# Kernel tuning notes

Hardware: AMD Instinct MI355X
Metric: run time of the kernel (lower is better)

Reference implementation:

```python
import jax, jax.numpy as jnp
import numpy as np

B, N, E, HD = 4, 2048, 2048, 128
E2 = 2 * E
EPS = 1e-6


def setup_inputs() -> dict:
    key = jax.random.key(0)
    ks = jax.random.split(key, 7)
    s = 0.02  # init_std
    return {
        "x": jax.random.normal(ks[0], (B, N, E), dtype=jnp.float32),
        "Wq1": jax.random.normal(ks[1], (E, HD), dtype=jnp.float32) * s,
        "Wq2": jax.random.normal(ks[2], (HD, E2), dtype=jnp.float32) * s,
        "Wk1": jax.random.normal(ks[3], (E, HD), dtype=jnp.float32) * s,
        "Wk2": jax.random.normal(ks[4], (HD, E2), dtype=jnp.float32) * s,
        "Wv": jax.random.normal(ks[5], (E, E2), dtype=jnp.float32) * s,
        "Wo": jax.random.normal(ks[6], (E2, E), dtype=jnp.float32) * s,
        "norm_w": jnp.ones((E2,), dtype=jnp.float32),
    }


def reference(x, Wq1, Wq2, Wk1, Wk2, Wv, Wo, norm_w):
    # low-rank factored projections: embed -> head_dim -> 2*embed
    q = jax.nn.silu((x @ Wq1) @ Wq2)          # [B,N,2E]
    log_f_raw = (x @ Wk1) @ Wk2                # [B,N,2E]
    v = x @ Wv                                 # [B,N,2E]

    # faithful to source (lower_bound is None branch):
    # f = sigmoid(raw); log_f = logsigmoid(f); k = 1 - exp(log_f)
    f = jax.nn.sigmoid(log_f_raw)
    log_f = jax.nn.log_sigmoid(f)
    a = jnp.exp(log_f)                         # decay (forget gate)
    k = 1.0 - a                                # input gate

    # HGRN-1 elementwise gated recurrence: h_t = a_t*h_{t-1} + k_t*v_t
    def combine(c1, c2):
        a1, b1 = c1
        a2, b2 = c2
        return (a1 * a2, a2 * b1 + b2)

    _, h = jax.lax.associative_scan(combine, (a, k * v), axis=1)
    out = q * h                                # [B,N,2E]

    # RMSNorm over channel dim (2E)
    out = out * jax.lax.rsqrt(jnp.mean(out * out, axis=-1, keepdims=True) + EPS)
    out = out * norm_w

    return out @ Wo                            # [B,N,E]
```

## Files before the change

### kernel.cpp

```cpp
#include <hip/hip_runtime.h>


typedef unsigned short u16;
typedef __attribute__((ext_vector_type(4))) float f32x4;
typedef __attribute__((ext_vector_type(8))) __bf16 bf16x8;
typedef __attribute__((ext_vector_type(8))) u16 u16x8;
typedef __attribute__((ext_vector_type(4))) unsigned int u32x4;

__device__ __forceinline__ float bf2f(u16 u) {
  unsigned int i = ((unsigned int)u) << 16;
  return __builtin_bit_cast(float, i);
}
__device__ __forceinline__ u16 f2bf(float f) {
  unsigned int i = __builtin_bit_cast(unsigned int, f);
  i += 0x7fffu + ((i >> 16) & 1u);
  return (u16)(i >> 16);
}

__device__ __forceinline__ void gload_lds16(const u16* g, u16* l) {
  __builtin_amdgcn_global_load_lds(
      (const __attribute__((address_space(1))) void*)g,
      (__attribute__((address_space(3))) void*)l, 16, 0, 0);
}

__global__ __launch_bounds__(256) void cast_kernel(const float* __restrict__ in,
                                                   u16* __restrict__ out, long n) {
  long i = ((long)blockIdx.x * 256 + threadIdx.x) * 4;
  if (i >= n) return;
  f32x4 fv = *(const f32x4*)&in[i];
  unsigned long long pk = (unsigned long long)f2bf(fv[0]) |
                          ((unsigned long long)f2bf(fv[1]) << 16) |
                          ((unsigned long long)f2bf(fv[2]) << 32) |
                          ((unsigned long long)f2bf(fv[3]) << 48);
  *(unsigned long long*)&out[i] = pk;
}

__global__ __launch_bounds__(256) void transpose_cast(const float* __restrict__ W,
                                                      u16* __restrict__ WT, int R, int Cc) {
  __shared__ float tile[32][33];
  const int tx = threadIdx.x, ty = threadIdx.y;
  const int x = blockIdx.x * 32 + tx;
  const int ybase = blockIdx.y * 32;
#pragma unroll
  for (int i = 0; i < 32; i += 8)
    tile[ty + i][tx] = W[(size_t)(ybase + ty + i) * Cc + x];
  __syncthreads();
  const int xt = ybase + tx;
  const int ytbase = blockIdx.x * 32;
#pragma unroll
  for (int i = 0; i < 32; i += 8)
    WT[(size_t)(ytbase + ty + i) * R + xt] = f2bf(tile[tx][ty + i]);
}

__global__ __launch_bounds__(256) void transpose_cast_nw(const float* __restrict__ W,
                                                         const float* __restrict__ nw,
                                                         u16* __restrict__ WT, int R, int Cc) {
  __shared__ float tile[32][33];
  const int tx = threadIdx.x, ty = threadIdx.y;
  const int x = blockIdx.x * 32 + tx;
  const int ybase = blockIdx.y * 32;
#pragma unroll
  for (int i = 0; i < 32; i += 8)
    tile[ty + i][tx] = W[(size_t)(ybase + ty + i) * Cc + x];
  __syncthreads();
  const int xt = ybase + tx;
  const float s = nw[xt];
  const int ytbase = blockIdx.x * 32;
#pragma unroll
  for (int i = 0; i < 32; i += 8)
    WT[(size_t)(ytbase + ty + i) * R + xt] = f2bf(tile[tx][ty + i] * s);
}

template <int EPI>
__global__ __launch_bounds__(256) void gemm_bt(const u16* __restrict__ A, int lda,
                                               const u16* __restrict__ BT,
                                               void* __restrict__ Cv,
                                               int M, int N, int K) {
  __shared__ __align__(16) u16 As[4096];
  __shared__ __align__(16) u16 Bs[4096];
  const int tid = threadIdx.x;
  const int lane = tid & 63;
  const int wid = tid >> 6;
  const int wr = wid >> 1, wc = wid & 1;
  const long bm = (long)blockIdx.x * 128;
  const long bn = (long)blockIdx.y * 128;

  const int sm = lane >> 2;
  const int sk = (lane & 3) << 3;
  const u16* Ag0 = A + (size_t)(bm + wid * 16 + sm) * lda + sk;
  const u16* Ag1 = A + (size_t)(bm + 64 + wid * 16 + sm) * lda + sk;
  const u16* Bg0 = BT + (size_t)(bn + wid * 16 + sm) * K + sk;
  const u16* Bg1 = BT + (size_t)(bn + 64 + wid * 16 + sm) * K + sk;
  u16* As0 = As + wid * 512;
  u16* As1 = As + 2048 + wid * 512;
  u16* Bs0 = Bs + wid * 512;
  u16* Bs1 = Bs + 2048 + wid * 512;

  f32x4 acc[4][4] = {};

  const int fra = wr * 64 + (lane & 15);
  const int frb = wc * 64 + (lane & 15);
  const int kg = (lane >> 4) << 3;

  for (int kk = 0; kk < K; kk += 32) {
    gload_lds16(Ag0 + kk, As0);
    gload_lds16(Ag1 + kk, As1);
    gload_lds16(Bg0 + kk, Bs0);
    gload_lds16(Bg1 + kk, Bs1);
    __syncthreads();
    bf16x8 af[4], bv[4];
#pragma unroll
    for (int mi = 0; mi < 4; ++mi)
      af[mi] = *reinterpret_cast<const bf16x8*>(&As[(fra + mi * 16) * 32 + kg]);
#pragma unroll
    for (int ni = 0; ni < 4; ++ni)
      bv[ni] = *reinterpret_cast<const bf16x8*>(&Bs[(frb + ni * 16) * 32 + kg]);
#pragma unroll
    for (int mi = 0; mi < 4; ++mi) {
#pragma unroll
      for (int ni = 0; ni < 4; ++ni)
        acc[mi][ni] =
            __builtin_amdgcn_mfma_f32_16x16x32_bf16(af[mi], bv[ni], acc[mi][ni], 0, 0, 0);
    }
    __syncthreads();
  }

  const int r0 = wr * 64 + ((lane >> 4) << 2);
  const int c0 = wc * 64 + (lane & 15);
#pragma unroll
  for (int mi = 0; mi < 4; ++mi) {
#pragma unroll
    for (int ni = 0; ni < 4; ++ni) {
#pragma unroll
      for (int r = 0; r < 4; ++r) {
        size_t row = (size_t)(bm + r0 + mi * 16 + r);
        size_t col = (size_t)(bn + c0 + ni * 16);
        size_t idx = row * (size_t)N + col;
        float val = acc[mi][ni][r];
        if constexpr (EPI == 0) {
          ((u16*)Cv)[idx] = f2bf(val);
        } else if constexpr (EPI == 2) {
          float f = 1.f / (1.f + __expf(-val));
          float aa = 1.f / (1.f + __expf(-f));
          ((u16*)Cv)[idx] = f2bf(aa);
        } else {
          float hv = bf2f(((u16*)Cv)[idx]);
          float s = 1.f / (1.f + __expf(-val));
          ((u16*)Cv)[idx] = f2bf(val * s * hv);
        }
      }
    }
  }
}

template <int EPI>
__global__ __launch_bounds__(512, 2) void gemm8(const u16* __restrict__ A,
                                                const u16* __restrict__ BT,
                                                void* __restrict__ Cv,
                                                const float* __restrict__ RS,
                                                int M, int N, int K, int nbx) {
  __shared__ __align__(16) u16 lds_[2][2][256][64];
  const int tid = threadIdx.x;
  const int lane = tid & 63;
  const int w = tid >> 6;
  const int wr = w >> 2;
  const int wc = w & 3;

  const int nwg = gridDim.x;
  const int bid = blockIdx.x;
  const int swz = (bid & 7) * (nwg >> 3) + (bid >> 3);
  const long bm = (long)(swz % nbx) * 256;
  const long bn = (long)(swz / nbx) * 256;

  const int sr = lane >> 3;
  const int sc = ((lane & 7) ^ sr) << 3;
  const u16* Ag = A + (size_t)(bm + w * 32 + sr) * K + sc;
  const u16* Bg = BT + (size_t)(bn + w * 32 + sr) * K + sc;

#define STAGE8(dbuf, t)                                              \
  {                                                                  \
    const u16* ag_ = Ag + (size_t)(t) * 64;                          \
    const u16* bg_ = Bg + (size_t)(t) * 64;                          \
    u16* la_ = &lds_[dbuf][0][w * 32][0];                            \
    u16* lb_ = &lds_[dbuf][1][w * 32][0];                            \
    gload_lds16(ag_, la_);                                           \
    gload_lds16(bg_, lb_);                                           \
    gload_lds16(ag_ + (size_t)8 * K, la_ + 512);                     \
    gload_lds16(bg_ + (size_t)8 * K, lb_ + 512);                     \
    gload_lds16(ag_ + (size_t)16 * K, la_ + 1024);                   \
    gload_lds16(bg_ + (size_t)16 * K, lb_ + 1024);                   \
    gload_lds16(ag_ + (size_t)24 * K, la_ + 1536);                   \
    gload_lds16(bg_ + (size_t)24 * K, lb_ + 1536);                   \
  }

  const int frow = lane & 15;
  const int fk8 = (lane >> 4) << 3;
  const int swz8 = (lane & 7) << 3;
  const int cr0 = fk8 ^ swz8;
  const int cr1 = (32 + fk8) ^ swz8;

  f32x4 acc[8][4] = {};

  STAGE8(0, 0);
  STAGE8(1, 1);
  asm volatile("s_waitcnt vmcnt(8)" ::: "memory");
  asm volatile("s_barrier" ::: "memory");

  const int NT = K >> 6;
  int cur = 0;
  for (int t = 0; t < NT; ++t) {
    const u16* LA = &lds_[cur][0][0][0];
    const u16* LB = &lds_[cur][1][0][0];
    bf16x8 af[4], bf_[4], ag2[4];
#pragma unroll
    for (int i = 0; i < 4; ++i)
      af[i] = *reinterpret_cast<const bf16x8*>(&LA[(wr * 128 + i * 16 + frow) * 64 + cr0]);
#pragma unroll
    for (int i = 0; i < 4; ++i)
      bf_[i] = *reinterpret_cast<const bf16x8*>(&LB[(wc * 64 + i * 16 + frow) * 64 + cr0]);
    __builtin_amdgcn_s_setprio(1);
#pragma unroll
    for (int i = 0; i < 4; ++i)
#pragma unroll
      for (int j = 0; j < 4; ++j)
        acc[i][j] = __builtin_amdgcn_mfma_f32_16x16x32_bf16(af[i], bf_[j], acc[i][j], 0, 0, 0);
    __builtin_amdgcn_s_setprio(0);
    asm volatile("s_barrier" ::: "memory");
#pragma unroll
    for (int i = 0; i < 4; ++i)
      ag2[i] = *reinterpret_cast<const bf16x8*>(&LA[(wr * 128 + 64 + i * 16 + frow) * 64 + cr0]);
    __builtin_amdgcn_s_setprio(1);
#pragma unroll
    for (int i = 0; i < 4; ++i)
#pragma unroll
      for (int j = 0; j < 4; ++j)
        acc[4 + i][j] = __builtin_amdgcn_mfma_f32_16x16x32_bf16(ag2[i], bf_[j], acc[4 + i][j], 0, 0, 0);
    __builtin_amdgcn_s_setprio(0);
    asm volatile("s_barrier" ::: "memory");
#pragma unroll
    for (int i = 0; i < 4; ++i)
      af[i] = *reinterpret_cast<const bf16x8*>(&LA[(wr * 128 + i * 16 + frow) * 64 + cr1]);
#pragma unroll
    for (int i = 0; i < 4; ++i)
      bf_[i] = *reinterpret_cast<const bf16x8*>(&LB[(wc * 64 + i * 16 + frow) * 64 + cr1]);
    __builtin_amdgcn_s_setprio(1);
#pragma unroll
    for (int i = 0; i < 4; ++i)
#pragma unroll
      for (int j = 0; j < 4; ++j)
        acc[i][j] = __builtin_amdgcn_mfma_f32_16x16x32_bf16(af[i], bf_[j], acc[i][j], 0, 0, 0);
    __builtin_amdgcn_s_setprio(0);
    asm volatile("s_barrier" ::: "memory");
#pragma unroll
    for (int i = 0; i < 4; ++i)
      ag2[i] = *reinterpret_cast<const bf16x8*>(&LA[(wr * 128 + 64 + i * 16 + frow) * 64 + cr1]);
    __builtin_amdgcn_s_setprio(1);
#pragma unroll
    for (int i = 0; i < 4; ++i)
#pragma unroll
      for (int j = 0; j < 4; ++j)
        acc[4 + i][j] = __builtin_amdgcn_mfma_f32_16x16x32_bf16(ag2[i], bf_[j], acc[4 + i][j], 0, 0, 0);
    __builtin_amdgcn_s_setprio(0);
    asm volatile("s_barrier" ::: "memory");

    if (t + 2 < NT) {
      STAGE8(cur, t + 2);
      asm volatile("s_waitcnt vmcnt(8)" ::: "memory");
    } else {
      asm volatile("s_waitcnt vmcnt(0)" ::: "memory");
    }
    asm volatile("s_barrier" ::: "memory");
    cur ^= 1;
  }

  const int er = (lane >> 4) << 2;
  const int ec = lane & 15;
#pragma unroll
  for (int mf = 0; mf < 8; ++mf) {
#pragma unroll
    for (int r = 0; r < 4; ++r) {
      const size_t row = (size_t)(bm + wr * 128 + mf * 16 + er + r);
      float rscale = 1.f;
      if constexpr (EPI == 3) rscale = RS[row];
#pragma unroll
      for (int nf = 0; nf < 4; ++nf) {
        const size_t col = (size_t)(bn + wc * 64 + nf * 16 + ec);
        const size_t idx = row * (size_t)N + col;
        const float val = acc[mf][nf][r];
        if constexpr (EPI == 0) {
          ((u16*)Cv)[idx] = f2bf(val);
        } else {
          ((float*)Cv)[idx] = val * rscale;
        }
      }
    }
  }
#undef STAGE8
}

__global__ __launch_bounds__(256) void scan_a(const u16* __restrict__ a,
                                              const u16* __restrict__ v,
                                              float* __restrict__ S_p,
                                              float* __restrict__ S_h) {
  const int idx = blockIdx.x * 256 + threadIdx.x;
  const int ch8 = idx & 511;
  const int c = (idx >> 9) & 31;
  const int b = idx >> 14;
  const int ch = ch8 << 3;
  size_t off = ((size_t)(b * 2048 + c * 64)) * 4096 + ch;
  float h[8], p[8];
#pragma unroll
  for (int j = 0; j < 8; ++j) { h[j] = 0.f; p[j] = 1.f; }
  for (int t = 0; t < 64; ++t) {
    u16x8 ua = *(const u16x8*)&a[off];
    u16x8 uv = *(const u16x8*)&v[off];
#pragma unroll
    for (int j = 0; j < 8; ++j) {
      float at = bf2f(ua[j]);
      h[j] = at * h[j] + (1.f - at) * bf2f(uv[j]);
      p[j] *= at;
    }
    off += 4096;
  }
  size_t so = (size_t)(b * 32 + c) * 4096 + ch;
#pragma unroll
  for (int j = 0; j < 8; ++j) { S_p[so + j] = p[j]; S_h[so + j] = h[j]; }
}

__global__ __launch_bounds__(256) void scan_b(const float* __restrict__ S_p,
                                              const float* __restrict__ S_h,
                                              float* __restrict__ Hin) {
  const int idx = blockIdx.x * 256 + threadIdx.x;
  const int b = idx >> 12;
  const int ch = idx & 4095;
  float H = 0.f;
  for (int c = 0; c < 32; ++c) {
    size_t so = (size_t)(b * 32 + c) * 4096 + ch;
    Hin[so] = H;
    H = S_p[so] * H + S_h[so];
  }
}

__global__ __launch_bounds__(256) void scan_c(const u16* __restrict__ a,
                                              u16* __restrict__ vh,
                                              const float* __restrict__ Hin) {
  const int idx = blockIdx.x * 256 + threadIdx.x;
  const int ch8 = idx & 511;
  const int c = (idx >> 9) & 31;
  const int b = idx >> 14;
  const int ch = ch8 << 3;
  size_t so = (size_t)(b * 32 + c) * 4096 + ch;
  float h[8];
#pragma unroll
  for (int j = 0; j < 8; ++j) h[j] = Hin[so + j];
  size_t off = ((size_t)(b * 2048 + c * 64)) * 4096 + ch;
  for (int t = 0; t < 64; ++t) {
    u16x8 ua = *(const u16x8*)&a[off];
    u16x8 uv = *(const u16x8*)&vh[off];
    u16x8 out;
#pragma unroll
    for (int j = 0; j < 8; ++j) {
      float at = bf2f(ua[j]);
      h[j] = at * h[j] + (1.f - at) * bf2f(uv[j]);
      out[j] = f2bf(h[j]);
    }
    *(u16x8*)&vh[off] = out;
    off += 4096;
  }
}

__global__ __launch_bounds__(256) void rowssq(const u16* __restrict__ g,
                                              float* __restrict__ rs) {
  const size_t base = (size_t)blockIdx.x * 4096;
  const int tid = threadIdx.x;
  const int c0 = tid * 16;
  u16 vals[16];
  *(u32x4*)&vals[0] = *(const u32x4*)&g[base + c0];
  *(u32x4*)&vals[8] = *(const u32x4*)&g[base + c0 + 8];
  float s = 0.f;
#pragma unroll
  for (int i = 0; i < 16; ++i) {
    float f = bf2f(vals[i]);
    s += f * f;
  }
#pragma unroll
  for (int o = 32; o > 0; o >>= 1) s += __shfl_down(s, o, 64);
  __shared__ float red[4];
  if ((tid & 63) == 0) red[tid >> 6] = s;
  __syncthreads();
  if (tid == 0) {
    float tot = red[0] + red[1] + red[2] + red[3];
    rs[blockIdx.x] = rsqrtf(tot * (1.0f / 4096.0f) + 1e-6f);
  }
}

extern "C" void kernel_launch(void* const* d_in, const int* in_sizes, int n_in,
                              void* d_out, int out_size, void* d_ws, size_t ws_size,
                              hipStream_t stream) {
  const float* x   = (const float*)d_in[0];
  const float* Wq1 = (const float*)d_in[1];
  const float* Wq2 = (const float*)d_in[2];
  const float* Wk1 = (const float*)d_in[3];
  const float* Wk2 = (const float*)d_in[4];
  const float* Wv  = (const float*)d_in[5];
  const float* Wo  = (const float*)d_in[6];
  const float* nw  = (const float*)d_in[7];

  char* ws = (char*)d_ws;
  u16* X     = (u16*)(ws + 0);
  u16* WVT   = (u16*)(ws + 33554432);
  u16* AA    = (u16*)(ws + 0);
  u16* VV    = (u16*)(ws + 67108864);
  u16* T12   = (u16*)(ws + 134217728);
  u16* WQK1T = (u16*)(ws + 138412032);
  u16* WQ2T  = (u16*)(ws + 139460608);
  u16* WK2T  = (u16*)(ws + 140509184);
  u16* WOT   = (u16*)(ws + 141557760);
  float* S_P = (float*)(ws + 158334976);
  float* S_H = (float*)(ws + 160432128);
  float* HIN = (float*)(ws + 162529280);
  float* RS  = (float*)(ws + 164626432);

  cast_kernel<<<16384, 256, 0, stream>>>(x, X, 16777216L);
  transpose_cast<<<dim3(4, 64),   dim3(32, 8), 0, stream>>>(Wq1, WQK1T, 2048, 128);
  transpose_cast<<<dim3(4, 64),   dim3(32, 8), 0, stream>>>(Wk1, WQK1T + 128 * 2048, 2048, 128);
  transpose_cast<<<dim3(128, 4),  dim3(32, 8), 0, stream>>>(Wq2, WQ2T, 128, 4096);
  transpose_cast<<<dim3(128, 4),  dim3(32, 8), 0, stream>>>(Wk2, WK2T, 128, 4096);
  transpose_cast<<<dim3(128, 64), dim3(32, 8), 0, stream>>>(Wv, WVT, 2048, 4096);
  transpose_cast_nw<<<dim3(64, 128), dim3(32, 8), 0, stream>>>(Wo, nw, WOT, 4096, 2048);

  gemm_bt<0><<<dim3(64, 2), 256, 0, stream>>>(X, 2048, WQK1T, T12, 8192, 256, 2048);
  gemm8<0><<<512, 512, 0, stream>>>(X, WVT, VV, nullptr, 8192, 4096, 2048, 32);
  gemm_bt<2><<<dim3(64, 32), 256, 0, stream>>>(T12 + 128, 256, WK2T, AA, 8192, 4096, 128);

  scan_a<<<256, 256, 0, stream>>>(AA, VV, S_P, S_H);
  scan_b<<<64, 256, 0, stream>>>(S_P, S_H, HIN);
  scan_c<<<256, 256, 0, stream>>>(AA, VV, HIN);

  gemm_bt<4><<<dim3(64, 32), 256, 0, stream>>>(T12, 256, WQ2T, VV, 8192, 4096, 128);

  rowssq<<<8192, 256, 0, stream>>>(VV, RS);
  gemm8<3><<<256, 512, 0, stream>>>(VV, WOT, d_out, RS, 8192, 2048, 4096, 32);
}
```

Baseline: 674.3 us.

## Restructure gemm8 into 4-stage K=32 pipeline with interleaved A/B staging

Rewrites the main bf16 GEMM loop: the K tile shrinks from 64 to 32 and the ring buffer grows from 2 to 4 stages in the same LDS footprint. A and B loads for step u+3 are now issued between the MFMA phases rather than all at the end of the iteration. The LDS XOR swizzle changes to fit 32-wide rows, and the tile mapping changes from column-major to row-major block order (nbx becomes nby). The aim is to keep more global loads in flight and overlap them with MFMA work, at the cost of more barriers per unit of K.

```diff
diff --git a/kernel.cpp b/kernel.cpp
--- a/kernel.cpp
+++ b/kernel.cpp
@@ -158,8 +158,8 @@
                                                 const u16* __restrict__ BT,
                                                 void* __restrict__ Cv,
                                                 const float* __restrict__ RS,
-                                                int M, int N, int K, int nbx) {
-  __shared__ __align__(16) u16 lds_[2][2][256][64];
+                                                int M, int N, int K, int nby) {
+  __shared__ __align__(16) u16 lds_[4][2][256][32];
   const int tid = threadIdx.x;
   const int lane = tid & 63;
   const int w = tid >> 6;
@@ -169,108 +169,76 @@
   const int nwg = gridDim.x;
   const int bid = blockIdx.x;
   const int swz = (bid & 7) * (nwg >> 3) + (bid >> 3);
-  const long bm = (long)(swz % nbx) * 256;
-  const long bn = (long)(swz / nbx) * 256;
-
-  const int sr = lane >> 3;
-  const int sc = ((lane & 7) ^ sr) << 3;
-  const u16* Ag = A + (size_t)(bm + w * 32 + sr) * K + sc;
-  const u16* Bg = BT + (size_t)(bn + w * 32 + sr) * K + sc;
-
-#define STAGE8(dbuf, t)                                              \
+  const long bm = (long)(swz / nby) * 256;
+  const long bn = (long)(swz % nby) * 256;
+
+  const int srow = lane >> 2;
+  const int scol = ((lane & 3) ^ ((lane >> 3) & 3)) << 3;
+  const u16* Ag = A + (size_t)(bm + w * 32 + srow) * K + scol;
+  const u16* Bg = BT + (size_t)(bn + w * 32 + srow) * K + scol;
+
+#define STG_A(t)                                                     \
   {                                                                  \
-    const u16* ag_ = Ag + (size_t)(t) * 64;                          \
-    const u16* bg_ = Bg + (size_t)(t) * 64;                          \
-    u16* la_ = &lds_[dbuf][0][w * 32][0];                            \
-    u16* lb_ = &lds_[dbuf][1][w * 32][0];                            \
-    gload_lds16(ag_, la_);                                           \
-    gload_lds16(bg_, lb_);                                           \
-    gload_lds16(ag_ + (size_t)8 * K, la_ + 512);                     \
-    gload_lds16(bg_ + (size_t)8 * K, lb_ + 512);                     \
-    gload_lds16(ag_ + (size_t)16 * K, la_ + 1024);                   \
-    gload_lds16(bg_ + (size_t)16 * K, lb_ + 1024);                   \
-    gload_lds16(ag_ + (size_t)24 * K, la_ + 1536);                   \
-    gload_lds16(bg_ + (size_t)24 * K, lb_ + 1536);                   \
+    const u16* s_ = Ag + (size_t)(t) * 32;                           \
+    u16* d_ = &lds_[(t) & 3][0][w * 32][0];                          \
+    gload_lds16(s_, d_);                                             \
+    gload_lds16(s_ + (size_t)16 * K, d_ + 512);                      \
+  }
+#define STG_B(t)                                                     \
+  {                                                                  \
+    const u16* s_ = Bg + (size_t)(t) * 32;                           \
+    u16* d_ = &lds_[(t) & 3][1][w * 32][0];                          \
+    gload_lds16(s_, d_);                                             \
+    gload_lds16(s_ + (size_t)16 * K, d_ + 512);                      \
   }
 
   const int frow = lane & 15;
-  const int fk8 = (lane >> 4) << 3;
-  const int swz8 = (lane & 7) << 3;
-  const int cr0 = fk8 ^ swz8;
-  const int cr1 = (32 + fk8) ^ swz8;
+  const int colw = (((lane >> 4) ^ ((frow >> 1) & 3)) << 3);
 
   f32x4 acc[8][4] = {};
 
-  STAGE8(0, 0);
-  STAGE8(1, 1);
-  asm volatile("s_waitcnt vmcnt(8)" ::: "memory");
-  asm volatile("s_barrier" ::: "memory");
-
-  const int NT = K >> 6;
-  int cur = 0;
-  for (int t = 0; t < NT; ++t) {
-    const u16* LA = &lds_[cur][0][0][0];
-    const u16* LB = &lds_[cur][1][0][0];
-    bf16x8 af[4], bf_[4], ag2[4];
+  const int NT = K >> 5;
+  STG_A(0); STG_B(0);
+  STG_A(1); STG_B(1);
+  STG_A(2); STG_B(2);
+
+  for (int u = 0; u < NT; ++u) {
+    const u16* LA = &lds_[u & 3][0][0][0];
+    const u16* LB = &lds_[u & 3][1][0][0];
+    asm volatile("s_waitcnt vmcnt(8)" ::: "memory");
+    __builtin_amdgcn_s_barrier();
+    bf16x8 a0[4], b0[4], a1[4];
 #pragma unroll
     for (int i = 0; i < 4; ++i)
-      af[i] = *reinterpret_cast<const bf16x8*>(&LA[(wr * 128 + i * 16 + frow) * 64 + cr0]);
+      a0[i] = *reinterpret_cast<const bf16x8*>(&LA[(wr * 128 + i * 16 + frow) * 32 + colw]);
 #pragma unroll
     for (int i = 0; i < 4; ++i)
-      bf_[i] = *reinterpret_cast<const bf16x8*>(&LB[(wc * 64 + i * 16 + frow) * 64 + cr0]);
+      b0[i] = *reinterpret_cast<const bf16x8*>(&LB[(wc * 64 + i * 16 + frow) * 32 + colw]);
+    if (u + 3 < NT) STG_A(u + 3);
+    __builtin_amdgcn_s_barrier();
+    asm volatile("s_waitcnt lgkmcnt(0)" ::: "memory");
     __builtin_amdgcn_s_setprio(1);
 #pragma unroll
     for (int i = 0; i < 4; ++i)
 #pragma unroll
       for (int j = 0; j < 4; ++j)
-        acc[i][j] = __builtin_amdgcn_mfma_f32_16x16x32_bf16(af[i], bf_[j], acc[i][j], 0, 0, 0);
+        acc[i][j] = __builtin_amdgcn_mfma_f32_16x16x32_bf16(a0[i], b0[j], acc[i][j], 0, 0, 0);
     __builtin_amdgcn_s_setprio(0);
-    asm volatile("s_barrier" ::: "memory");
+    __builtin_amdgcn_s_barrier();
 #pragma unroll
     for (int i = 0; i < 4; ++i)
-      ag2[i] = *reinterpret_cast<const bf16x8*>(&LA[(wr * 128 + 64 + i * 16 + frow) * 64 + cr0]);
+      a1[i] = *reinterpret_cast<const bf16x8*>(&LA[(wr * 128 + 64 + i * 16 + frow) * 32 + colw]);
+    if (u + 3 < NT) STG_B(u + 3);
+    __builtin_amdgcn_s_barrier();
+    asm volatile("s_waitcnt lgkmcnt(0)" ::: "memory");
     __builtin_amdgcn_s_setprio(1);
 #pragma unroll
     for (int i = 0; i < 4; ++i)
 #pragma unroll
       for (int j = 0; j < 4; ++j)
-        acc[4 + i][j] = __builtin_amdgcn_mfma_f32_16x16x32_bf16(ag2[i], bf_[j], acc[4 + i][j], 0, 0, 0);
+        acc[4 + i][j] = __builtin_amdgcn_mfma_f32_16x16x32_bf16(a1[i], b0[j], acc[4 + i][j], 0, 0, 0);
     __builtin_amdgcn_s_setprio(0);
-    asm volatile("s_barrier" ::: "memory");
-#pragma unroll
-    for (int i = 0; i < 4; ++i)
-      af[i] = *reinterpret_cast<const bf16x8*>(&LA[(wr * 128 + i * 16 + frow) * 64 + cr1]);
-#pragma unroll
-    for (int i = 0; i < 4; ++i)
-      bf_[i] = *reinterpret_cast<const bf16x8*>(&LB[(wc * 64 + i * 16 + frow) * 64 + cr1]);
-    __builtin_amdgcn_s_setprio(1);
-#pragma unroll
-    for (int i = 0; i < 4; ++i)
-#pragma unroll
-      for (int j = 0; j < 4; ++j)
-        acc[i][j] = __builtin_amdgcn_mfma_f32_16x16x32_bf16(af[i], bf_[j], acc[i][j], 0, 0, 0);
-    __builtin_amdgcn_s_setprio(0);
-    asm volatile("s_barrier" ::: "memory");
-#pragma unroll
-    for (int i = 0; i < 4; ++i)
-      ag2[i] = *reinterpret_cast<const bf16x8*>(&LA[(wr * 128 + 64 + i * 16 + frow) * 64 + cr1]);
-    __builtin_amdgcn_s_setprio(1);
-#pragma unroll
-    for (int i = 0; i < 4; ++i)
-#pragma unroll
-      for (int j = 0; j < 4; ++j)
-        acc[4 + i][j] = __builtin_amdgcn_mfma_f32_16x16x32_bf16(ag2[i], bf_[j], acc[4 + i][j], 0, 0, 0);
-    __builtin_amdgcn_s_setprio(0);
-    asm volatile("s_barrier" ::: "memory");
-
-    if (t + 2 < NT) {
-      STAGE8(cur, t + 2);
-      asm volatile("s_waitcnt vmcnt(8)" ::: "memory");
-    } else {
-      asm volatile("s_waitcnt vmcnt(0)" ::: "memory");
-    }
-    asm volatile("s_barrier" ::: "memory");
-    cur ^= 1;
+    __builtin_amdgcn_s_barrier();
   }
 
   const int er = (lane >> 4) << 2;
@@ -295,7 +263,8 @@
       }
     }
   }
-#undef STAGE8
+#undef STG_A
+#undef STG_B
 }
 
 __global__ __launch_bounds__(256) void scan_a(const u16* __restrict__ a,
@@ -430,7 +399,7 @@
   transpose_cast_nw<<<dim3(64, 128), dim3(32, 8), 0, stream>>>(Wo, nw, WOT, 4096, 2048);
 
   gemm_bt<0><<<dim3(64, 2), 256, 0, stream>>>(X, 2048, WQK1T, T12, 8192, 256, 2048);
-  gemm8<0><<<512, 512, 0, stream>>>(X, WVT, VV, nullptr, 8192, 4096, 2048, 32);
+  gemm8<0><<<512, 512, 0, stream>>>(X, WVT, VV, nullptr, 8192, 4096, 2048, 16);
   gemm_bt<2><<<dim3(64, 32), 256, 0, stream>>>(T12 + 128, 256, WK2T, AA, 8192, 4096, 128);
 
   scan_a<<<256, 256, 0, stream>>>(AA, VV, S_P, S_H);
@@ -440,5 +409,5 @@
   gemm_bt<4><<<dim3(64, 32), 256, 0, stream>>>(T12, 256, WQ2T, VV, 8192, 4096, 128);
 
   rowssq<<<8192, 256, 0, stream>>>(VV, RS);
-  gemm8<3><<<256, 512, 0, stream>>>(VV, WOT, d_out, RS, 8192, 2048, 4096, 32);
-}
+  gemm8<3><<<256, 512, 0, stream>>>(VV, WOT, d_out, RS, 8192, 2048, 4096, 8);
+}
```

New measurement: 665.8 us. No clear change (-1.3%).
